# Kernel tuning notes

Hardware: AMD Instinct MI355X
Metric: run time of the kernel (lower is better)

## Reference

```python
import jax, jax.numpy as jnp
import numpy as np

REFRACTORY_PERIOD = 5
DAMPENING_FACTOR = 0.3


def setup_inputs() -> dict:
    key = jax.random.key(0)
    B, T, N = 32, 4096, 256
    x = jax.random.normal(key, (B, T, N), dtype=jnp.float32)
    return {"x": x}


def _refractory_scan(x):
    # x: [B, T, N]; scan over time keeping refractory counter q resident.
    B, T, N = x.shape
    xt = jnp.swapaxes(x, 0, 1)  # [T, B, N]

    def step(q, x_t):
        cond = (x_t > 0) & (q == 0)
        z_t = jnp.where(cond, jnp.ones_like(q), jnp.zeros_like(q))
        q = jnp.maximum(jnp.zeros_like(q), q - 1) + REFRACTORY_PERIOD * z_t
        return q, z_t

    q0 = jnp.zeros((B, N), dtype=x.dtype)
    # Note: the t=0 case in the original (z0 = x0>0, q = R*z0) is exactly the
    # first step of this scan starting from q0 = 0.
    _, z = jax.lax.scan(step, q0, xt)
    return jnp.swapaxes(z, 0, 1)  # [B, T, N]


def reference(x) -> jnp.ndarray:
    # Forward value is exactly z_forward (the surrogate-gradient straight-through
    # construction leaves the value unchanged).
    return _refractory_scan(x)
```

## Files before the change

### kernel.cpp

```cpp
#include <hip/hip_runtime.h>
#include <cstdint>
#include <cstddef>

#define BB 32
#define TT 4096
#define NNV 64
#define CC 32
#define PSUB 16
#define PG 8
#define NCH 256

__device__ __forceinline__ uint32_t tbl_from_mask(uint32_t m) {
    uint32_t tbl = 0;
    #pragma unroll
    for (int e = 0; e < 6; ++e) {
        int na = e;
        #pragma unroll
        for (int it = 0; it < 6; ++it) {
            const uint32_t r = (na < 32) ? (m >> na) : 0u;
            const int t = na + (r ? __builtin_ctz(r) : 0);
            na = r ? (t + 6) : na;
        }
        const int q = na > CC ? na - CC : 0;
        tbl |= (uint32_t)q << (4 * e);
    }
    return tbl;
}

__global__ __launch_bounds__(1024, 4) void refrac_fused(const float* __restrict__ x,
                                                        float* __restrict__ z,
                                                        uint8_t* __restrict__ msg) {
    const int tid = threadIdx.x;
    const int pg = blockIdx.x >> 5;
    const int b  = blockIdx.x & 31;
    const int psub = tid >> 6;
    const int n4 = tid & 63;
    const int p = pg * PSUB + psub;

    const float4* __restrict__ xv = reinterpret_cast<const float4*>(x)
        + ((size_t)b * TT + (size_t)p * CC) * NNV + n4;

    uint32_t cur[4] = {0u, 0u, 0u, 0u};
    #pragma unroll
    for (int jb = 0; jb < CC; jb += 8) {
        float4 buf[8];
        #pragma unroll
        for (int u = 0; u < 8; ++u)
            buf[u] = xv[(size_t)(jb + u) * NNV];
        #pragma unroll
        for (int u = 0; u < 8; ++u) {
            const int j = jb + u;
            cur[0] |= (buf[u].x > 0.0f) ? (1u << j) : 0u;
            cur[1] |= (buf[u].y > 0.0f) ? (1u << j) : 0u;
            cur[2] |= (buf[u].z > 0.0f) ? (1u << j) : 0u;
            cur[3] |= (buf[u].w > 0.0f) ? (1u << j) : 0u;
        }
    }

    __shared__ uint32_t tbl_lds[PSUB][NCH];
    __shared__ uint8_t  ent_lds[PSUB][NCH];

    #pragma unroll
    for (int c = 0; c < 4; ++c)
        tbl_lds[psub][n4 * 4 + c] = tbl_from_mask(cur[c]);
    __syncthreads();

    if (tid < NCH) {
        const int n = tid;
        uint32_t t16[PSUB];
        #pragma unroll
        for (int s = 0; s < PSUB; ++s) t16[s] = tbl_lds[s][n];

        int e = 0;
        if (pg > 0) {
            const uint8_t* inb = msg + (((size_t)b * PG + (pg - 1)) << 8) + n;
            uint32_t v;
            while ((v = __hip_atomic_load(inb, __ATOMIC_RELAXED,
                                          __HIP_MEMORY_SCOPE_AGENT)) & 0x80u)
                __builtin_amdgcn_s_sleep(1);
            e = (int)(v & 0xFu);
        }
        #pragma unroll
        for (int s = 0; s < PSUB; ++s) {
            ent_lds[s][n] = (uint8_t)e;
            e = (int)((t16[s] >> (4 * e)) & 0xFu);
        }
        if (pg < PG - 1)
            __hip_atomic_store(msg + (((size_t)b * PG + pg) << 8) + n,
                               (uint8_t)e, __ATOMIC_RELAXED,
                               __HIP_MEMORY_SCOPE_AGENT);
    }
    __syncthreads();

    float4* __restrict__ zv = reinterpret_cast<float4*>(z)
        + ((size_t)b * TT + (size_t)p * CC) * NNV + n4;

    const uint32_t e4 = *reinterpret_cast<const uint32_t*>(&ent_lds[psub][n4 * 4]);
    uint32_t spk[4];
    #pragma unroll
    for (int c = 0; c < 4; ++c) {
        const uint32_t m = cur[c];
        int na = (int)((e4 >> (8 * c)) & 0xFFu);
        uint32_t s = 0;
        #pragma unroll
        for (int it = 0; it < 6; ++it) {
            const uint32_t r = (na < 32) ? (m >> na) : 0u;
            const int t = na + (r ? __builtin_ctz(r) : 0);
            s |= r ? (1u << (t & 31)) : 0u;
            na = r ? (t + 6) : na;
        }
        spk[c] = s;
    }

    #pragma unroll
    for (int j = 0; j < CC; ++j) {
        float4 o;
        o.x = ((spk[0] >> j) & 1u) ? 1.0f : 0.0f;
        o.y = ((spk[1] >> j) & 1u) ? 1.0f : 0.0f;
        o.z = ((spk[2] >> j) & 1u) ? 1.0f : 0.0f;
        o.w = ((spk[3] >> j) & 1u) ? 1.0f : 0.0f;
        zv[(size_t)j * NNV] = o;
    }
}

extern "C" void kernel_launch(void* const* d_in, const int* in_sizes, int n_in,
                              void* d_out, int out_size, void* d_ws, size_t ws_size,
                              hipStream_t stream) {
    const float* x = (const float*)d_in[0];
    float* z = (float*)d_out;
    uint8_t* msg = (uint8_t*)d_ws;

    hipMemsetAsync(d_ws, 0xAA, (size_t)BB * PG * NCH, stream);

    refrac_fused<<<dim3(BB * PG), 1024, 0, stream>>>(x, z, msg);
}
```

Before: 235.4 us.

## Replace inter-block chained scan with in-block parallel prefix over transition tables

Each block now owns a 16-channel slice of one batch over the whole time axis, so there is no cross-block message passing or spin-waiting. The entry states of the 128 time chunks come from a log-step Hillis-Steele scan of 6-state transition tables composed in LDS. The memset of the workspace is removed, and the output is written with nontemporal stores. The cost is more composition work and seven barrier steps, and each thread's loads now span only 64 contiguous bytes per row, which reduces coalescing width.

```diff
diff --git a/kernel.cpp b/kernel.cpp
--- a/kernel.cpp
+++ b/kernel.cpp
@@ -5,10 +5,23 @@
 #define BB 32
 #define TT 4096
 #define NNV 64
+#define SLW 4
+#define NSL 16
 #define CC 32
-#define PSUB 16
-#define PG 8
-#define NCH 256
+#define NCK 128
+#define NCHB 16
+
+typedef float f32x4 __attribute__((ext_vector_type(4)));
+
+__device__ __forceinline__ uint32_t comp6(uint32_t f, uint32_t g) {
+    uint32_t h = 0;
+    #pragma unroll
+    for (int e = 0; e < 6; ++e) {
+        const uint32_t fe = (f >> (4 * e)) & 0xFu;
+        h |= ((g >> (4 * fe)) & 0xFu) << (4 * e);
+    }
+    return h;
+}
 
 __device__ __forceinline__ uint32_t tbl_from_mask(uint32_t m) {
     uint32_t tbl = 0;
@@ -27,18 +40,16 @@
     return tbl;
 }
 
-__global__ __launch_bounds__(1024, 4) void refrac_fused(const float* __restrict__ x,
-                                                        float* __restrict__ z,
-                                                        uint8_t* __restrict__ msg) {
+__global__ __launch_bounds__(512, 4) void refrac(const float* __restrict__ x,
+                                                 float* __restrict__ z) {
     const int tid = threadIdx.x;
-    const int pg = blockIdx.x >> 5;
-    const int b  = blockIdx.x & 31;
-    const int psub = tid >> 6;
-    const int n4 = tid & 63;
-    const int p = pg * PSUB + psub;
+    const int b  = blockIdx.x >> 4;
+    const int ns = blockIdx.x & (NSL - 1);
+    const int n4r = tid & (SLW - 1);
+    const int ck  = tid >> 2;
 
     const float4* __restrict__ xv = reinterpret_cast<const float4*>(x)
-        + ((size_t)b * TT + (size_t)p * CC) * NNV + n4;
+        + ((size_t)b * TT + (size_t)ck * CC) * NNV + ns * SLW + n4r;
 
     uint32_t cur[4] = {0u, 0u, 0u, 0u};
     #pragma unroll
@@ -57,50 +68,35 @@
         }
     }
 
-    __shared__ uint32_t tbl_lds[PSUB][NCH];
-    __shared__ uint8_t  ent_lds[PSUB][NCH];
-
+    __shared__ uint32_t sc[2][NCK][NCHB];
     #pragma unroll
     for (int c = 0; c < 4; ++c)
-        tbl_lds[psub][n4 * 4 + c] = tbl_from_mask(cur[c]);
+        sc[0][ck][n4r * 4 + c] = tbl_from_mask(cur[c]);
     __syncthreads();
 
-    if (tid < NCH) {
-        const int n = tid;
-        uint32_t t16[PSUB];
+    int sb = 0;
+    #pragma unroll
+    for (int o = 1; o < NCK; o <<= 1) {
         #pragma unroll
-        for (int s = 0; s < PSUB; ++s) t16[s] = tbl_lds[s][n];
+        for (int it = 0; it < (NCK * NCHB) / 512; ++it) {
+            const int i  = tid + it * 512;
+            const int ic = i >> 4;
+            const int ch = i & (NCHB - 1);
+            uint32_t v = sc[sb][ic][ch];
+            if (ic >= o) v = comp6(sc[sb][ic - o][ch], v);
+            sc[sb ^ 1][ic][ch] = v;
+        }
+        __syncthreads();
+        sb ^= 1;
+    }
 
-        int e = 0;
-        if (pg > 0) {
-            const uint8_t* inb = msg + (((size_t)b * PG + (pg - 1)) << 8) + n;
-            uint32_t v;
-            while ((v = __hip_atomic_load(inb, __ATOMIC_RELAXED,
-                                          __HIP_MEMORY_SCOPE_AGENT)) & 0x80u)
-                __builtin_amdgcn_s_sleep(1);
-            e = (int)(v & 0xFu);
-        }
-        #pragma unroll
-        for (int s = 0; s < PSUB; ++s) {
-            ent_lds[s][n] = (uint8_t)e;
-            e = (int)((t16[s] >> (4 * e)) & 0xFu);
-        }
-        if (pg < PG - 1)
-            __hip_atomic_store(msg + (((size_t)b * PG + pg) << 8) + n,
-                               (uint8_t)e, __ATOMIC_RELAXED,
-                               __HIP_MEMORY_SCOPE_AGENT);
-    }
-    __syncthreads();
-
-    float4* __restrict__ zv = reinterpret_cast<float4*>(z)
-        + ((size_t)b * TT + (size_t)p * CC) * NNV + n4;
-
-    const uint32_t e4 = *reinterpret_cast<const uint32_t*>(&ent_lds[psub][n4 * 4]);
     uint32_t spk[4];
     #pragma unroll
     for (int c = 0; c < 4; ++c) {
+        const int e0 = (ck == 0) ? 0
+            : (int)(sc[sb][ck - 1][n4r * 4 + c] & 0xFu);
         const uint32_t m = cur[c];
-        int na = (int)((e4 >> (8 * c)) & 0xFFu);
+        int na = e0;
         uint32_t s = 0;
         #pragma unroll
         for (int it = 0; it < 6; ++it) {
@@ -112,14 +108,16 @@
         spk[c] = s;
     }
 
+    f32x4* __restrict__ zv = reinterpret_cast<f32x4*>(z)
+        + ((size_t)b * TT + (size_t)ck * CC) * NNV + ns * SLW + n4r;
+
     #pragma unroll
     for (int j = 0; j < CC; ++j) {
-        float4 o;
-        o.x = ((spk[0] >> j) & 1u) ? 1.0f : 0.0f;
-        o.y = ((spk[1] >> j) & 1u) ? 1.0f : 0.0f;
-        o.z = ((spk[2] >> j) & 1u) ? 1.0f : 0.0f;
-        o.w = ((spk[3] >> j) & 1u) ? 1.0f : 0.0f;
-        zv[(size_t)j * NNV] = o;
+        f32x4 o = { ((spk[0] >> j) & 1u) ? 1.0f : 0.0f,
+                    ((spk[1] >> j) & 1u) ? 1.0f : 0.0f,
+                    ((spk[2] >> j) & 1u) ? 1.0f : 0.0f,
+                    ((spk[3] >> j) & 1u) ? 1.0f : 0.0f };
+        __builtin_nontemporal_store(o, &zv[(size_t)j * NNV]);
     }
 }
 
@@ -128,9 +126,7 @@
                               hipStream_t stream) {
     const float* x = (const float*)d_in[0];
     float* z = (float*)d_out;
-    uint8_t* msg = (uint8_t*)d_ws;
+    (void)d_ws; (void)ws_size;
 
-    hipMemsetAsync(d_ws, 0xAA, (size_t)BB * PG * NCH, stream);
-
-    refrac_fused<<<dim3(BB * PG), 1024, 0, stream>>>(x, z, msg);
+    refrac<<<dim3(BB * NSL), 512, 0, stream>>>(x, z);
 }
```

Measured after the change: 273.0 us. +16.0%, slower.

## Publish composed state maps per chunk group instead of serial carry chain

Applied to the files above, without the earlier changes.

Each block now composes its 16 per-subchunk transition tables into one 6-state map and publishes it right away, without first waiting on the previous group's exit state. Downstream blocks wait for all earlier groups' maps and apply them in sequence to get their entry state. This replaces a serial chain of cross-block dependencies with a decoupled-lookback style scheme. In exchange, the message buffer grows to 32-bit entries and each block polls up to seven predecessors.

```diff
diff --git a/kernel.cpp b/kernel.cpp
--- a/kernel.cpp
+++ b/kernel.cpp
@@ -9,6 +9,16 @@
 #define PSUB 16
 #define PG 8
 #define NCH 256
+
+__device__ __forceinline__ uint32_t comp6(uint32_t f, uint32_t g) {
+    uint32_t h = 0;
+    #pragma unroll
+    for (int e = 0; e < 6; ++e) {
+        const uint32_t fe = (f >> (4 * e)) & 0xFu;
+        h |= ((g >> (4 * fe)) & 0xFu) << (4 * e);
+    }
+    return h;
+}
 
 __device__ __forceinline__ uint32_t tbl_from_mask(uint32_t m) {
     uint32_t tbl = 0;
@@ -29,7 +39,7 @@
 
 __global__ __launch_bounds__(1024, 4) void refrac_fused(const float* __restrict__ x,
                                                         float* __restrict__ z,
-                                                        uint8_t* __restrict__ msg) {
+                                                        uint32_t* __restrict__ msg) {
     const int tid = threadIdx.x;
     const int pg = blockIdx.x >> 5;
     const int b  = blockIdx.x & 31;
@@ -71,24 +81,45 @@
         #pragma unroll
         for (int s = 0; s < PSUB; ++s) t16[s] = tbl_lds[s][n];
 
+        if (pg < PG - 1) {
+            uint32_t map = t16[0];
+            #pragma unroll
+            for (int s = 1; s < PSUB; ++s) map = comp6(map, t16[s]);
+            __hip_atomic_store(msg + (((size_t)b * PG + pg) << 8) + n, map,
+                               __ATOMIC_RELAXED, __HIP_MEMORY_SCOPE_AGENT);
+        }
+
+        uint32_t mv[PG - 1];
+        #pragma unroll
+        for (int g = 0; g < PG - 1; ++g) mv[g] = 0x80000000u;
+        if (pg > 0) {
+            const uint32_t* base = msg + (((size_t)b * PG) << 8) + n;
+            for (;;) {
+                bool ok = true;
+                #pragma unroll
+                for (int g = 0; g < PG - 1; ++g) {
+                    if (g < pg && (mv[g] & 0x80000000u)) {
+                        mv[g] = __hip_atomic_load(base + ((size_t)g << 8),
+                                                  __ATOMIC_RELAXED,
+                                                  __HIP_MEMORY_SCOPE_AGENT);
+                        ok &= !(mv[g] & 0x80000000u);
+                    }
+                }
+                if (ok) break;
+                __builtin_amdgcn_s_sleep(1);
+            }
+        }
+
         int e = 0;
-        if (pg > 0) {
-            const uint8_t* inb = msg + (((size_t)b * PG + (pg - 1)) << 8) + n;
-            uint32_t v;
-            while ((v = __hip_atomic_load(inb, __ATOMIC_RELAXED,
-                                          __HIP_MEMORY_SCOPE_AGENT)) & 0x80u)
-                __builtin_amdgcn_s_sleep(1);
-            e = (int)(v & 0xFu);
-        }
+        #pragma unroll
+        for (int g = 0; g < PG - 1; ++g)
+            if (g < pg) e = (int)((mv[g] >> (4 * e)) & 0xFu);
+
         #pragma unroll
         for (int s = 0; s < PSUB; ++s) {
             ent_lds[s][n] = (uint8_t)e;
             e = (int)((t16[s] >> (4 * e)) & 0xFu);
         }
-        if (pg < PG - 1)
-            __hip_atomic_store(msg + (((size_t)b * PG + pg) << 8) + n,
-                               (uint8_t)e, __ATOMIC_RELAXED,
-                               __HIP_MEMORY_SCOPE_AGENT);
     }
     __syncthreads();
 
@@ -128,9 +159,9 @@
                               hipStream_t stream) {
     const float* x = (const float*)d_in[0];
     float* z = (float*)d_out;
-    uint8_t* msg = (uint8_t*)d_ws;
+    uint32_t* msg = (uint32_t*)d_ws;
 
-    hipMemsetAsync(d_ws, 0xAA, (size_t)BB * PG * NCH, stream);
+    hipMemsetAsync(d_ws, 0xAA, (size_t)BB * PG * NCH * sizeof(uint32_t), stream);
 
     refrac_fused<<<dim3(BB * PG), 1024, 0, stream>>>(x, z, msg);
 }
```

New measurement: 235.4 us. About the same (+0.0%).
